# Kernel optimization log

Hardware: AMD Instinct MI355X
Metric: run time of the kernel (lower is better)

## Reference

```python
import jax, jax.numpy as jnp
import numpy as np

B, C, H, W = 16, 512, 64, 64
C8 = C // 8
MAX_LEN = 512


def setup_inputs() -> dict:
    key = jax.random.key(0)
    ks = jax.random.split(key, 9)
    s = 0.05
    return {
        "x": jax.random.normal(ks[0], (B, C, H, W), dtype=jnp.float32),
        "Wq": jax.random.normal(ks[1], (C8, C), dtype=jnp.float32) * s,
        "bq": jax.random.normal(ks[2], (C8,), dtype=jnp.float32) * s,
        "Wk": jax.random.normal(ks[3], (C8, C), dtype=jnp.float32) * s,
        "bk": jax.random.normal(ks[4], (C8,), dtype=jnp.float32) * s,
        "Wv": jax.random.normal(ks[5], (C, C), dtype=jnp.float32) * s,
        "bv": jax.random.normal(ks[6], (C,), dtype=jnp.float32) * s,
        "rel_h": jax.random.normal(ks[7], (C8, MAX_LEN), dtype=jnp.float32),
        "rel_w": jax.random.normal(ks[8], (C8, MAX_LEN), dtype=jnp.float32),
    }


def reference(x, Wq, bq, Wk, bk, Wv, bv, rel_h, rel_w):
    # 1x1 convs == per-pixel channel matmuls
    q = jnp.einsum('bchw,oc->bohw', x, Wq) + bq[None, :, None, None]  # [B,C8,H,W]
    k = jnp.einsum('bchw,oc->bohw', x, Wk) + bk[None, :, None, None]  # [B,C8,H,W]
    v = jnp.einsum('bchw,oc->bohw', x, Wv) + bv[None, :, None, None]  # [B,C,H,W]
    # relative position added directly to Q (per-row) and K (per-column)
    q = q + rel_h[None, :, :H, None]   # broadcast over width
    k = k + rel_w[None, :, None, :W]   # broadcast over height
    # axial attention over the width axis: scores [B,H,W,W]
    attn = jnp.einsum('bchw,bchv->bhwv', q, k)
    attn = jax.nn.softmax(attn, axis=-1)
    # AV: out[b,d,h,w] = sum_v attn[b,h,w,v] * value[b,d,h,v]
    out = jnp.einsum('bhwv,bdhv->bdhw', attn, v)
    return out
```

## Files before the change

### kernel.cpp

```cpp
#include <hip/hip_runtime.h>


#define BDIM 512

typedef __attribute__((ext_vector_type(8))) short bf16x8;
typedef __attribute__((ext_vector_type(4))) float f32x4;

__device__ __forceinline__ unsigned short f2bf(float f){
  union { float f; unsigned u; } v; v.f = f;
  unsigned r = v.u + 0x7FFFu + ((v.u >> 16) & 1u);
  return (unsigned short)(r >> 16);
}
__device__ __forceinline__ float bf2f(unsigned short b){
  union { unsigned u; float f; } v; v.u = ((unsigned)b) << 16; return v.f;
}

#define MFMA16(a, b, c) __builtin_amdgcn_mfma_f32_16x16x32_bf16((a), (b), (c), 0, 0, 0)

__global__ void convert_w(const float* __restrict__ Wq, const float* __restrict__ Wk,
                          const float* __restrict__ Wv, unsigned short* __restrict__ wsw){
  const int stride = gridDim.x * blockDim.x;
  const int t0 = blockIdx.x * blockDim.x + threadIdx.x;
  for (int t = t0; t < 32768; t += stride){
    float f = Wq[t]; unsigned short h = f2bf(f);
    wsw[t] = h; wsw[32768 + t] = f2bf(f - bf2f(h));
    f = Wk[t]; h = f2bf(f);
    wsw[65536 + t] = h; wsw[98304 + t] = f2bf(f - bf2f(h));
  }
  for (int t = t0; t < 262144; t += stride)
    wsw[131072 + t] = f2bf(Wv[t]);
}

template<bool WS>
__global__ __launch_bounds__(BDIM)
void axial_attn(const float* __restrict__ x,
                const float* __restrict__ bq, const float* __restrict__ bk,
                const float* __restrict__ bv,
                const float* __restrict__ rel_h, const float* __restrict__ rel_w,
                const float* __restrict__ Wq, const float* __restrict__ Wk,
                const float* __restrict__ Wv,
                const unsigned short* __restrict__ wsw,
                float* __restrict__ out)
{
  extern __shared__ char smem[];
  unsigned short* const xhi = (unsigned short*)smem;
  char* const RB = smem + 66560;
  unsigned short* const xlo = (unsigned short*)RB;
  unsigned short* const wqh = (unsigned short*)(RB + 17408);
  unsigned short* const wql = (unsigned short*)(RB + 34816);
  unsigned short* const wkh = (unsigned short*)(RB + 52224);
  unsigned short* const wkl = (unsigned short*)(RB + 69632);
  unsigned short* const Qh  = (unsigned short*)RB;
  unsigned short* const Ql  = (unsigned short*)(RB + 9216);
  unsigned short* const Kh  = (unsigned short*)(RB + 18432);
  unsigned short* const Kl  = (unsigned short*)(RB + 27648);
  unsigned short* const att = (unsigned short*)(RB + 77824);
  unsigned short* const wvb = (unsigned short*)RB;
  unsigned short* const Vt  = (unsigned short*)(RB + 66560);

  const int bid = blockIdx.x;
  const int b = bid >> 6, h = bid & 63;
  const int tid = threadIdx.x;
  const int wave = tid >> 6, lane = tid & 63;
  const int lg = lane >> 4, li = lane & 15;
  const int mt = wave >> 1;
  const int npair = (wave & 1) * 2;

  const f32x4 z4 = {0.f, 0.f, 0.f, 0.f};
  f32x4 accQ[2] = {z4, z4}, accK[2] = {z4, z4};

  for (int cc = 0; cc < 4; ++cc){
    const int c0 = cc * 128;
    {
      const int w4 = (tid & 15) * 4;
      const int cb = tid >> 4;
      #pragma unroll
      for (int it = 0; it < 4; ++it){
        const int cl = cb + it * 32;
        const float4 v = *(const float4*)(x + (((b * 512 + c0 + cl) * 64 + h) * 64 + w4));
        const float ff[4] = {v.x, v.y, v.z, v.w};
        #pragma unroll
        for (int j = 0; j < 4; ++j){
          const unsigned short hi = f2bf(ff[j]);
          xhi[(w4 + j) * 520 + c0 + cl] = hi;
          xlo[(w4 + j) * 136 + cl] = f2bf(ff[j] - bf2f(hi));
        }
      }
    }
    if (WS){
      #pragma unroll
      for (int bi = 0; bi < 4; ++bi){
        unsigned short* const dst = (bi==0)?wqh:(bi==1)?wql:(bi==2)?wkh:wkl;
        const unsigned short* const src = wsw + bi * 32768;
        #pragma unroll
        for (int it = 0; it < 2; ++it){
          const int idx = tid + it * BDIM;
          const int o = idx >> 4, j8 = (idx & 15) * 8;
          *(int4*)(dst + o * 136 + j8) = *(const int4*)(src + o * 512 + c0 + j8);
        }
      }
    } else {
      #pragma unroll
      for (int mi = 0; mi < 2; ++mi){
        const float* const src = mi ? Wk : Wq;
        unsigned short* const dh = mi ? wkh : wqh;
        unsigned short* const dl = mi ? wkl : wql;
        #pragma unroll
        for (int it = 0; it < 2; ++it){
          const int idx = tid + it * BDIM;
          const int o = idx >> 4, j8 = (idx & 15) * 8;
          const float* const s2 = src + o * 512 + c0 + j8;
          const float4 f0 = *(const float4*)s2, f1 = *(const float4*)(s2 + 4);
          const float ff[8] = {f0.x,f0.y,f0.z,f0.w,f1.x,f1.y,f1.z,f1.w};
          union { unsigned short s[8]; int4 v; } ph, pl;
          #pragma unroll
          for (int j = 0; j < 8; ++j){
            ph.s[j] = f2bf(ff[j]);
            pl.s[j] = f2bf(ff[j] - bf2f(ph.s[j]));
          }
          *(int4*)(dh + o * 136 + j8) = ph.v;
          *(int4*)(dl + o * 136 + j8) = pl.v;
        }
      }
    }
    __syncthreads();
    const int arow = (mt * 16 + li) * 520 + c0;
    const int lrow = (mt * 16 + li) * 136;
    #pragma unroll
    for (int ks = 0; ks < 4; ++ks){
      const int ko = ks * 32 + lg * 8;
      const bf16x8 ah = *(const bf16x8*)(xhi + arow + ko);
      const bf16x8 al = *(const bf16x8*)(xlo + lrow + ko);
      #pragma unroll
      for (int nj = 0; nj < 2; ++nj){
        const int orow = ((npair + nj) * 16 + li) * 136 + ko;
        const bf16x8 bhq = *(const bf16x8*)(wqh + orow);
        const bf16x8 blq = *(const bf16x8*)(wql + orow);
        const bf16x8 bhk = *(const bf16x8*)(wkh + orow);
        const bf16x8 blk = *(const bf16x8*)(wkl + orow);
        accQ[nj] = MFMA16(ah, bhq, accQ[nj]);
        accQ[nj] = MFMA16(ah, blq, accQ[nj]);
        accQ[nj] = MFMA16(al, bhq, accQ[nj]);
        accK[nj] = MFMA16(ah, bhk, accK[nj]);
        accK[nj] = MFMA16(ah, blk, accK[nj]);
        accK[nj] = MFMA16(al, bhk, accK[nj]);
      }
    }
    __syncthreads();
  }

  #pragma unroll
  for (int nj = 0; nj < 2; ++nj){
    const int o = (npair + nj) * 16 + li;
    const float qb = bq[o] + rel_h[o * 512 + h];
    const float bko = bk[o];
    #pragma unroll
    for (int r = 0; r < 4; ++r){
      const int row = mt * 16 + lg * 4 + r;
      const float qv = accQ[nj][r] + qb;
      const unsigned short qhi = f2bf(qv);
      Qh[row * 72 + o] = qhi;
      Ql[row * 72 + o] = f2bf(qv - bf2f(qhi));
      const float kv = accK[nj][r] + bko + rel_w[o * 512 + row];
      const unsigned short khi = f2bf(kv);
      Kh[row * 72 + o] = khi;
      Kl[row * 72 + o] = f2bf(kv - bf2f(khi));
    }
  }
  __syncthreads();

  if (wave < 4){
    f32x4 s[4] = {z4, z4, z4, z4};
    #pragma unroll
    for (int ks = 0; ks < 2; ++ks){
      const int ko = ks * 32 + lg * 8;
      const bf16x8 aqh = *(const bf16x8*)(Qh + (wave * 16 + li) * 72 + ko);
      const bf16x8 aql = *(const bf16x8*)(Ql + (wave * 16 + li) * 72 + ko);
      #pragma unroll
      for (int nt = 0; nt < 4; ++nt){
        const bf16x8 bh = *(const bf16x8*)(Kh + (nt * 16 + li) * 72 + ko);
        const bf16x8 bl = *(const bf16x8*)(Kl + (nt * 16 + li) * 72 + ko);
        s[nt] = MFMA16(aqh, bh, s[nt]);
        s[nt] = MFMA16(aqh, bl, s[nt]);
        s[nt] = MFMA16(aql, bh, s[nt]);
      }
    }
    #pragma unroll
    for (int r = 0; r < 4; ++r){
      float mx = fmaxf(fmaxf(s[0][r], s[1][r]), fmaxf(s[2][r], s[3][r]));
      mx = fmaxf(mx, __shfl_xor(mx, 1));
      mx = fmaxf(mx, __shfl_xor(mx, 2));
      mx = fmaxf(mx, __shfl_xor(mx, 4));
      mx = fmaxf(mx, __shfl_xor(mx, 8));
      const float e0 = __expf(s[0][r] - mx), e1 = __expf(s[1][r] - mx);
      const float e2 = __expf(s[2][r] - mx), e3 = __expf(s[3][r] - mx);
      float sum = e0 + e1 + e2 + e3;
      sum += __shfl_xor(sum, 1); sum += __shfl_xor(sum, 2);
      sum += __shfl_xor(sum, 4); sum += __shfl_xor(sum, 8);
      const float inv = 1.f / sum;
      const int row = wave * 16 + lg * 4 + r;
      att[row * 72 +  0 + li] = f2bf(e0 * inv);
      att[row * 72 + 16 + li] = f2bf(e1 * inv);
      att[row * 72 + 32 + li] = f2bf(e2 * inv);
      att[row * 72 + 48 + li] = f2bf(e3 * inv);
    }
  }
  __syncthreads();

  for (int dc = 0; dc < 8; ++dc){
    const int d0 = dc * 64;
    if (WS){
      #pragma unroll
      for (int it = 0; it < 8; ++it){
        const int idx = tid + it * BDIM;
        const int d = idx >> 6, j8 = (idx & 63) * 8;
        *(int4*)(wvb + d * 520 + j8) =
          *(const int4*)(wsw + 131072 + (d0 + d) * 512 + j8);
      }
    } else {
      #pragma unroll
      for (int it = 0; it < 8; ++it){
        const int idx = tid + it * BDIM;
        const int d = idx >> 6, j8 = (idx & 63) * 8;
        const float* const s2 = Wv + (d0 + d) * 512 + j8;
        const float4 f0 = *(const float4*)s2, f1 = *(const float4*)(s2 + 4);
        const float ff[8] = {f0.x,f0.y,f0.z,f0.w,f1.x,f1.y,f1.z,f1.w};
        union { unsigned short s[8]; int4 v; } p;
        #pragma unroll
        for (int j = 0; j < 8; ++j) p.s[j] = f2bf(ff[j]);
        *(int4*)(wvb + d * 520 + j8) = p.v;
      }
    }
    __syncthreads();
    f32x4 accV[2] = {z4, z4};
    const int vrow = (mt * 16 + li) * 520;
    #pragma unroll
    for (int ks = 0; ks < 16; ++ks){
      const int ko = ks * 32 + lg * 8;
      const bf16x8 a = *(const bf16x8*)(xhi + vrow + ko);
      #pragma unroll
      for (int nj = 0; nj < 2; ++nj){
        const bf16x8 bb = *(const bf16x8*)(wvb + ((npair + nj) * 16 + li) * 520 + ko);
        accV[nj] = MFMA16(a, bb, accV[nj]);
      }
    }
    #pragma unroll
    for (int nj = 0; nj < 2; ++nj){
      const int d = (npair + nj) * 16 + li;
      const float bvd = bv[d0 + d];
      const int v0 = mt * 16 + lg * 4;
      union { unsigned short s[4]; uint2 v; } p;
      #pragma unroll
      for (int r = 0; r < 4; ++r) p.s[r] = f2bf(accV[nj][r] + bvd);
      *(uint2*)(Vt + d * 72 + v0) = p.v;
    }
    __syncthreads();
    f32x4 accO[2] = {z4, z4};
    #pragma unroll
    for (int ks = 0; ks < 2; ++ks){
      const int ko = ks * 32 + lg * 8;
      const bf16x8 a = *(const bf16x8*)(Vt + (mt * 16 + li) * 72 + ko);
      #pragma unroll
      for (int nj = 0; nj < 2; ++nj){
        const bf16x8 bb = *(const bf16x8*)(att + ((npair + nj) * 16 + li) * 72 + ko);
        accO[nj] = MFMA16(a, bb, accO[nj]);
      }
    }
    #pragma unroll
    for (int nj = 0; nj < 2; ++nj){
      const int wcol = (npair + nj) * 16 + li;
      #pragma unroll
      for (int r = 0; r < 4; ++r){
        const int d = d0 + mt * 16 + lg * 4 + r;
        out[((b * 512 + d) * 64 + h) * 64 + wcol] = accO[nj][r];
      }
    }
  }
}

extern "C" void kernel_launch(void* const* d_in, const int* in_sizes, int n_in,
                              void* d_out, int out_size, void* d_ws, size_t ws_size,
                              hipStream_t stream){
  const float* x     = (const float*)d_in[0];
  const float* Wq    = (const float*)d_in[1];
  const float* bq    = (const float*)d_in[2];
  const float* Wk    = (const float*)d_in[3];
  const float* bk    = (const float*)d_in[4];
  const float* Wv    = (const float*)d_in[5];
  const float* bv    = (const float*)d_in[6];
  const float* rel_h = (const float*)d_in[7];
  const float* rel_w = (const float*)d_in[8];
  float* out = (float*)d_out;

  const dim3 grid(1024), blk(BDIM);
  const size_t smem = 153600;

  if (ws_size >= 786432){
    convert_w<<<1024, 256, 0, stream>>>(Wq, Wk, Wv, (unsigned short*)d_ws);
    axial_attn<true><<<grid, blk, smem, stream>>>(x, bq, bk, bv, rel_h, rel_w,
                                                  Wq, Wk, Wv,
                                                  (const unsigned short*)d_ws, out);
  } else {
    axial_attn<false><<<grid, blk, smem, stream>>>(x, bq, bk, bv, rel_h, rel_w,
                                                   Wq, Wk, Wv, nullptr, out);
  }
}
```

Before: 389.1 us.

## Keep x fragments in registers and double-buffer Wv to shrink LDS footprint

```diff
diff --git a/kernel.cpp b/kernel.cpp
--- a/kernel.cpp
+++ b/kernel.cpp
@@ -16,6 +16,22 @@
 }
 
 #define MFMA16(a, b, c) __builtin_amdgcn_mfma_f32_16x16x32_bf16((a), (b), (c), 0, 0, 0)
+
+#define XH  0
+#define XL  4608
+#define WQH 9216
+#define WQL 13824
+#define WKH 18432
+#define WKL 23040
+#define QH  0
+#define QL  4608
+#define KH  9216
+#define KL  13824
+#define WVB0 0
+#define WVB1 16640
+#define VT   33280
+#define ATT  35584
+#define SMEM_BYTES 80384
 
 __global__ void convert_w(const float* __restrict__ Wq, const float* __restrict__ Wk,
                           const float* __restrict__ Wv, unsigned short* __restrict__ wsw){
@@ -32,7 +48,7 @@
 }
 
 template<bool WS>
-__global__ __launch_bounds__(BDIM)
+__global__ __launch_bounds__(BDIM, 4)
 void axial_attn(const float* __restrict__ x,
                 const float* __restrict__ bq, const float* __restrict__ bk,
                 const float* __restrict__ bv,
@@ -42,21 +58,7 @@
                 const unsigned short* __restrict__ wsw,
                 float* __restrict__ out)
 {
-  extern __shared__ char smem[];
-  unsigned short* const xhi = (unsigned short*)smem;
-  char* const RB = smem + 66560;
-  unsigned short* const xlo = (unsigned short*)RB;
-  unsigned short* const wqh = (unsigned short*)(RB + 17408);
-  unsigned short* const wql = (unsigned short*)(RB + 34816);
-  unsigned short* const wkh = (unsigned short*)(RB + 52224);
-  unsigned short* const wkl = (unsigned short*)(RB + 69632);
-  unsigned short* const Qh  = (unsigned short*)RB;
-  unsigned short* const Ql  = (unsigned short*)(RB + 9216);
-  unsigned short* const Kh  = (unsigned short*)(RB + 18432);
-  unsigned short* const Kl  = (unsigned short*)(RB + 27648);
-  unsigned short* const att = (unsigned short*)(RB + 77824);
-  unsigned short* const wvb = (unsigned short*)RB;
-  unsigned short* const Vt  = (unsigned short*)(RB + 66560);
+  extern __shared__ unsigned short S[];
 
   const int bid = blockIdx.x;
   const int b = bid >> 6, h = bid & 63;
@@ -64,80 +66,75 @@
   const int wave = tid >> 6, lane = tid & 63;
   const int lg = lane >> 4, li = lane & 15;
   const int mt = wave >> 1;
-  const int npair = (wave & 1) * 2;
+  const int nt = wave & 1;
+  const int npair = nt * 2;
 
   const f32x4 z4 = {0.f, 0.f, 0.f, 0.f};
   f32x4 accQ[2] = {z4, z4}, accK[2] = {z4, z4};
-
-  for (int cc = 0; cc < 4; ++cc){
-    const int c0 = cc * 128;
+  bf16x8 xa[16];
+
+  const int xw  = tid & 63;
+  const int xc8 = (tid >> 6) << 3;
+  const int wo  = tid >> 3;
+  const int wj8 = (tid & 7) << 3;
+
+  #pragma unroll
+  for (int cc = 0; cc < 8; ++cc){
+    const int c0 = cc << 6;
     {
-      const int w4 = (tid & 15) * 4;
-      const int cb = tid >> 4;
-      #pragma unroll
-      for (int it = 0; it < 4; ++it){
-        const int cl = cb + it * 32;
-        const float4 v = *(const float4*)(x + (((b * 512 + c0 + cl) * 64 + h) * 64 + w4));
-        const float ff[4] = {v.x, v.y, v.z, v.w};
+      const float* xp = x + (size_t)(b * 512 + c0 + xc8) * 4096 + h * 64 + xw;
+      float f[8];
+      #pragma unroll
+      for (int i = 0; i < 8; ++i) f[i] = xp[(size_t)i * 4096];
+      #pragma unroll
+      for (int half = 0; half < 2; ++half){
+        union { unsigned short s[4]; uint2 v; } ph, pl;
         #pragma unroll
         for (int j = 0; j < 4; ++j){
-          const unsigned short hi = f2bf(ff[j]);
-          xhi[(w4 + j) * 520 + c0 + cl] = hi;
-          xlo[(w4 + j) * 136 + cl] = f2bf(ff[j] - bf2f(hi));
+          const float ff = f[half * 4 + j];
+          ph.s[j] = f2bf(ff);
+          pl.s[j] = f2bf(ff - bf2f(ph.s[j]));
         }
+        *(uint2*)(S + XH + xw * 72 + xc8 + half * 4) = ph.v;
+        *(uint2*)(S + XL + xw * 72 + xc8 + half * 4) = pl.v;
       }
     }
     if (WS){
-      #pragma unroll
-      for (int bi = 0; bi < 4; ++bi){
-        unsigned short* const dst = (bi==0)?wqh:(bi==1)?wql:(bi==2)?wkh:wkl;
-        const unsigned short* const src = wsw + bi * 32768;
+      *(int4*)(S + WQH + wo * 72 + wj8) = *(const int4*)(wsw +     0 + wo * 512 + c0 + wj8);
+      *(int4*)(S + WQL + wo * 72 + wj8) = *(const int4*)(wsw + 32768 + wo * 512 + c0 + wj8);
+      *(int4*)(S + WKH + wo * 72 + wj8) = *(const int4*)(wsw + 65536 + wo * 512 + c0 + wj8);
+      *(int4*)(S + WKL + wo * 72 + wj8) = *(const int4*)(wsw + 98304 + wo * 512 + c0 + wj8);
+    } else {
+      #pragma unroll
+      for (int mi = 0; mi < 2; ++mi){
+        const float* src = (mi ? Wk : Wq) + wo * 512 + c0 + wj8;
+        const float4 f0 = *(const float4*)src, f1 = *(const float4*)(src + 4);
+        const float ff[8] = {f0.x,f0.y,f0.z,f0.w,f1.x,f1.y,f1.z,f1.w};
+        union { unsigned short s[8]; int4 v; } ph, pl;
         #pragma unroll
-        for (int it = 0; it < 2; ++it){
-          const int idx = tid + it * BDIM;
-          const int o = idx >> 4, j8 = (idx & 15) * 8;
-          *(int4*)(dst + o * 136 + j8) = *(const int4*)(src + o * 512 + c0 + j8);
+        for (int j = 0; j < 8; ++j){
+          ph.s[j] = f2bf(ff[j]);
+          pl.s[j] = f2bf(ff[j] - bf2f(ph.s[j]));
         }
-      }
-    } else {
-      #pragma unroll
-      for (int mi = 0; mi < 2; ++mi){
-        const float* const src = mi ? Wk : Wq;
-        unsigned short* const dh = mi ? wkh : wqh;
-        unsigned short* const dl = mi ? wkl : wql;
-        #pragma unroll
-        for (int it = 0; it < 2; ++it){
-          const int idx = tid + it * BDIM;
-          const int o = idx >> 4, j8 = (idx & 15) * 8;
-          const float* const s2 = src + o * 512 + c0 + j8;
-          const float4 f0 = *(const float4*)s2, f1 = *(const float4*)(s2 + 4);
-          const float ff[8] = {f0.x,f0.y,f0.z,f0.w,f1.x,f1.y,f1.z,f1.w};
-          union { unsigned short s[8]; int4 v; } ph, pl;
-          #pragma unroll
-          for (int j = 0; j < 8; ++j){
-            ph.s[j] = f2bf(ff[j]);
-            pl.s[j] = f2bf(ff[j] - bf2f(ph.s[j]));
-          }
-          *(int4*)(dh + o * 136 + j8) = ph.v;
-          *(int4*)(dl + o * 136 + j8) = pl.v;
-        }
+        *(int4*)(S + (mi ? WKH : WQH) + wo * 72 + wj8) = ph.v;
+        *(int4*)(S + (mi ? WKL : WQL) + wo * 72 + wj8) = pl.v;
       }
     }
     __syncthreads();
-    const int arow = (mt * 16 + li) * 520 + c0;
-    const int lrow = (mt * 16 + li) * 136;
-    #pragma unroll
-    for (int ks = 0; ks < 4; ++ks){
+    const int arow = (mt * 16 + li) * 72;
+    #pragma unroll
+    for (int ks = 0; ks < 2; ++ks){
       const int ko = ks * 32 + lg * 8;
-      const bf16x8 ah = *(const bf16x8*)(xhi + arow + ko);
-      const bf16x8 al = *(const bf16x8*)(xlo + lrow + ko);
+      const bf16x8 ah = *(const bf16x8*)(S + XH + arow + ko);
+      const bf16x8 al = *(const bf16x8*)(S + XL + arow + ko);
+      xa[cc * 2 + ks] = ah;
       #pragma unroll
       for (int nj = 0; nj < 2; ++nj){
-        const int orow = ((npair + nj) * 16 + li) * 136 + ko;
-        const bf16x8 bhq = *(const bf16x8*)(wqh + orow);
-        const bf16x8 blq = *(const bf16x8*)(wql + orow);
-        const bf16x8 bhk = *(const bf16x8*)(wkh + orow);
-        const bf16x8 blk = *(const bf16x8*)(wkl + orow);
+        const int brow = ((npair + nj) * 16 + li) * 72 + ko;
+        const bf16x8 bhq = *(const bf16x8*)(S + WQH + brow);
+        const bf16x8 blq = *(const bf16x8*)(S + WQL + brow);
+        const bf16x8 bhk = *(const bf16x8*)(S + WKH + brow);
+        const bf16x8 blk = *(const bf16x8*)(S + WKL + brow);
         accQ[nj] = MFMA16(ah, bhq, accQ[nj]);
         accQ[nj] = MFMA16(ah, blq, accQ[nj]);
         accQ[nj] = MFMA16(al, bhq, accQ[nj]);
@@ -159,12 +156,12 @@
       const int row = mt * 16 + lg * 4 + r;
       const float qv = accQ[nj][r] + qb;
       const unsigned short qhi = f2bf(qv);
-      Qh[row * 72 + o] = qhi;
-      Ql[row * 72 + o] = f2bf(qv - bf2f(qhi));
+      S[QH + row * 72 + o] = qhi;
+      S[QL + row * 72 + o] = f2bf(qv - bf2f(qhi));
       const float kv = accK[nj][r] + bko + rel_w[o * 512 + row];
       const unsigned short khi = f2bf(kv);
-      Kh[row * 72 + o] = khi;
-      Kl[row * 72 + o] = f2bf(kv - bf2f(khi));
+      S[KH + row * 72 + o] = khi;
+      S[KL + row * 72 + o] = f2bf(kv - bf2f(khi));
     }
   }
   __syncthreads();
@@ -174,15 +171,15 @@
     #pragma unroll
     for (int ks = 0; ks < 2; ++ks){
       const int ko = ks * 32 + lg * 8;
-      const bf16x8 aqh = *(const bf16x8*)(Qh + (wave * 16 + li) * 72 + ko);
-      const bf16x8 aql = *(const bf16x8*)(Ql + (wave * 16 + li) * 72 + ko);
-      #pragma unroll
-      for (int nt = 0; nt < 4; ++nt){
-        const bf16x8 bh = *(const bf16x8*)(Kh + (nt * 16 + li) * 72 + ko);
-        const bf16x8 bl = *(const bf16x8*)(Kl + (nt * 16 + li) * 72 + ko);
-        s[nt] = MFMA16(aqh, bh, s[nt]);
-        s[nt] = MFMA16(aqh, bl, s[nt]);
-        s[nt] = MFMA16(aql, bh, s[nt]);
+      const bf16x8 aqh = *(const bf16x8*)(S + QH + (wave * 16 + li) * 72 + ko);
+      const bf16x8 aql = *(const bf16x8*)(S + QL + (wave * 16 + li) * 72 + ko);
+      #pragma unroll
+      for (int ntt = 0; ntt < 4; ++ntt){
+        const bf16x8 bh = *(const bf16x8*)(S + KH + (ntt * 16 + li) * 72 + ko);
+        const bf16x8 bl = *(const bf16x8*)(S + KL + (ntt * 16 + li) * 72 + ko);
+        s[ntt] = MFMA16(aqh, bh, s[ntt]);
+        s[ntt] = MFMA16(aqh, bl, s[ntt]);
+        s[ntt] = MFMA16(aql, bh, s[ntt]);
       }
     }
     #pragma unroll
@@ -199,82 +196,90 @@
       sum += __shfl_xor(sum, 4); sum += __shfl_xor(sum, 8);
       const float inv = 1.f / sum;
       const int row = wave * 16 + lg * 4 + r;
-      att[row * 72 +  0 + li] = f2bf(e0 * inv);
-      att[row * 72 + 16 + li] = f2bf(e1 * inv);
-      att[row * 72 + 32 + li] = f2bf(e2 * inv);
-      att[row * 72 + 48 + li] = f2bf(e3 * inv);
+      S[ATT + row * 72 +  0 + li] = f2bf(e0 * inv);
+      S[ATT + row * 72 + 16 + li] = f2bf(e1 * inv);
+      S[ATT + row * 72 + 32 + li] = f2bf(e2 * inv);
+      S[ATT + row * 72 + 48 + li] = f2bf(e3 * inv);
     }
   }
   __syncthreads();
 
-  for (int dc = 0; dc < 8; ++dc){
-    const int d0 = dc * 64;
-    if (WS){
-      #pragma unroll
-      for (int it = 0; it < 8; ++it){
-        const int idx = tid + it * BDIM;
-        const int d = idx >> 6, j8 = (idx & 63) * 8;
-        *(int4*)(wvb + d * 520 + j8) =
-          *(const int4*)(wsw + 131072 + (d0 + d) * 512 + j8);
-      }
-    } else {
-      #pragma unroll
-      for (int it = 0; it < 8; ++it){
-        const int idx = tid + it * BDIM;
-        const int d = idx >> 6, j8 = (idx & 63) * 8;
-        const float* const s2 = Wv + (d0 + d) * 512 + j8;
-        const float4 f0 = *(const float4*)s2, f1 = *(const float4*)(s2 + 4);
+  auto loadWv = [&](int d0, int4* r){
+    #pragma unroll
+    for (int it = 0; it < 4; ++it){
+      const int idx = tid + it * BDIM;
+      const int d = idx >> 6, j8 = (idx & 63) << 3;
+      if (WS){
+        r[it] = *(const int4*)(wsw + 131072 + (d0 + d) * 512 + j8);
+      } else {
+        const float* src = Wv + (d0 + d) * 512 + j8;
+        const float4 f0 = *(const float4*)src, f1 = *(const float4*)(src + 4);
         const float ff[8] = {f0.x,f0.y,f0.z,f0.w,f1.x,f1.y,f1.z,f1.w};
         union { unsigned short s[8]; int4 v; } p;
         #pragma unroll
         for (int j = 0; j < 8; ++j) p.s[j] = f2bf(ff[j]);
-        *(int4*)(wvb + d * 520 + j8) = p.v;
-      }
+        r[it] = p.v;
+      }
+    }
+  };
+  auto writeWv = [&](int base, const int4* r){
+    #pragma unroll
+    for (int it = 0; it < 4; ++it){
+      const int idx = tid + it * BDIM;
+      const int d = idx >> 6, j8 = (idx & 63) << 3;
+      *(int4*)(S + base + d * 520 + j8) = r[it];
+    }
+  };
+
+  {
+    int4 r[4];
+    loadWv(0, r);
+    writeWv(WVB0, r);
+  }
+  __syncthreads();
+
+  for (int dc = 0; dc < 16; ++dc){
+    const int cur = dc & 1;
+    const int WB  = cur ? WVB1 : WVB0;
+    const int WBn = cur ? WVB0 : WVB1;
+    const bool pf = (dc < 15);
+    int4 r[4];
+    if (pf) loadWv((dc + 1) * 32, r);
+
+    f32x4 accV = z4;
+    const int bbase = (nt * 16 + li) * 520 + lg * 8;
+    #pragma unroll
+    for (int ks = 0; ks < 16; ++ks){
+      const bf16x8 bb = *(const bf16x8*)(S + WB + bbase + ks * 32);
+      accV = MFMA16(xa[ks], bb, accV);
+    }
+    if (pf) writeWv(WBn, r);
+
+    {
+      const int d = nt * 16 + li;
+      const float bvd = bv[dc * 32 + d];
+      union { unsigned short s[4]; uint2 v; } p;
+      #pragma unroll
+      for (int rr = 0; rr < 4; ++rr) p.s[rr] = f2bf(accV[rr] + bvd);
+      *(uint2*)(S + VT + d * 72 + mt * 16 + lg * 4) = p.v;
     }
     __syncthreads();
-    f32x4 accV[2] = {z4, z4};
-    const int vrow = (mt * 16 + li) * 520;
-    #pragma unroll
-    for (int ks = 0; ks < 16; ++ks){
-      const int ko = ks * 32 + lg * 8;
-      const bf16x8 a = *(const bf16x8*)(xhi + vrow + ko);
-      #pragma unroll
-      for (int nj = 0; nj < 2; ++nj){
-        const bf16x8 bb = *(const bf16x8*)(wvb + ((npair + nj) * 16 + li) * 520 + ko);
-        accV[nj] = MFMA16(a, bb, accV[nj]);
-      }
-    }
-    #pragma unroll
-    for (int nj = 0; nj < 2; ++nj){
-      const int d = (npair + nj) * 16 + li;
-      const float bvd = bv[d0 + d];
-      const int v0 = mt * 16 + lg * 4;
-      union { unsigned short s[4]; uint2 v; } p;
-      #pragma unroll
-      for (int r = 0; r < 4; ++r) p.s[r] = f2bf(accV[nj][r] + bvd);
-      *(uint2*)(Vt + d * 72 + v0) = p.v;
-    }
-    __syncthreads();
-    f32x4 accO[2] = {z4, z4};
+
+    f32x4 accO = z4;
     #pragma unroll
     for (int ks = 0; ks < 2; ++ks){
       const int ko = ks * 32 + lg * 8;
-      const bf16x8 a = *(const bf16x8*)(Vt + (mt * 16 + li) * 72 + ko);
-      #pragma unroll
-      for (int nj = 0; nj < 2; ++nj){
-        const bf16x8 bb = *(const bf16x8*)(att + ((npair + nj) * 16 + li) * 72 + ko);
-        accO[nj] = MFMA16(a, bb, accO[nj]);
-      }
-    }
-    #pragma unroll
-    for (int nj = 0; nj < 2; ++nj){
-      const int wcol = (npair + nj) * 16 + li;
-      #pragma unroll
-      for (int r = 0; r < 4; ++r){
-        const int d = d0 + mt * 16 + lg * 4 + r;
-        out[((b * 512 + d) * 64 + h) * 64 + wcol] = accO[nj][r];
-      }
-    }
+      const bf16x8 a  = *(const bf16x8*)(S + ATT + (mt * 16 + li) * 72 + ko);
+      const bf16x8 bb = *(const bf16x8*)(S + VT  + (nt * 16 + li) * 72 + ko);
+      accO = MFMA16(a, bb, accO);
+    }
+    {
+      const int d  = dc * 32 + nt * 16 + li;
+      const int w0 = mt * 16 + lg * 4;
+      float4 o4 = {accO[0], accO[1], accO[2], accO[3]};
+      *(float4*)(out + (size_t)(b * 512 + d) * 4096 + h * 64 + w0) = o4;
+    }
+    __syncthreads();
   }
 }
 
@@ -293,15 +298,14 @@
   float* out = (float*)d_out;
 
   const dim3 grid(1024), blk(BDIM);
-  const size_t smem = 153600;
 
   if (ws_size >= 786432){
     convert_w<<<1024, 256, 0, stream>>>(Wq, Wk, Wv, (unsigned short*)d_ws);
-    axial_attn<true><<<grid, blk, smem, stream>>>(x, bq, bk, bv, rel_h, rel_w,
-                                                  Wq, Wk, Wv,
-                                                  (const unsigned short*)d_ws, out);
+    axial_attn<true><<<grid, blk, SMEM_BYTES, stream>>>(x, bq, bk, bv, rel_h, rel_w,
+                                                        Wq, Wk, Wv,
+                                                        (const unsigned short*)d_ws, out);
   } else {
-    axial_attn<false><<<grid, blk, smem, stream>>>(x, bq, bk, bv, rel_h, rel_w,
-                                                   Wq, Wk, Wv, nullptr, out);
-  }
-}
+    axial_attn<false><<<grid, blk, SMEM_BYTES, stream>>>(x, bq, bk, bv, rel_h, rel_w,
+                                                         Wq, Wk, Wv, nullptr, out);
+  }
+}
```

New measurement: 379.1 us. 2.5% less time.
